# Optimization experiments

Measured on AMD Instinct MI355X. Metric: run time of the kernel, lower is better.

Reference implementation:

```python
import jax, jax.numpy as jnp
import numpy as np
import math

N = 100000      # num vertices
M = 50000       # num hyperedges
NNZ = 800000    # incidence entries
F_IN = 128
NHID = 128
NCLS = 40
DEPTH = 4
ALPHA = 0.1     # restart_alpha
LAMDA = 0.5


def setup_inputs() -> dict:
    key = jax.random.key(0)
    ks = jax.random.split(key, 8)
    x = jax.random.normal(ks[0], (N, F_IN), jnp.float32)
    vertex = jax.random.randint(ks[1], (NNZ,), 0, N)
    edges = jax.random.randint(ks[2], (NNZ,), 0, M)
    s0 = 1.0 / np.sqrt(F_IN)
    sh = 1.0 / np.sqrt(NHID)
    W0 = jax.random.uniform(ks[3], (F_IN, NHID), jnp.float32, -s0, s0)
    b0 = jax.random.uniform(ks[4], (NHID,), jnp.float32, -s0, s0)
    Ws = jax.random.uniform(ks[5], (DEPTH, NHID, NHID), jnp.float32, -sh, sh)
    Wout = jax.random.uniform(ks[6], (NHID, NCLS), jnp.float32, -sh, sh)
    bout = jax.random.uniform(ks[7], (NCLS,), jnp.float32, -sh, sh)
    return {"x": x, "W0": W0, "b0": b0, "Ws": Ws, "Wout": Wout,
            "bout": bout, "vertex": vertex, "edges": edges}


def reference(x, W0, b0, Ws, Wout, bout, vertex, edges):
    ones = jnp.ones((NNZ, 1), x.dtype)
    cnt_e = jnp.maximum(jax.ops.segment_sum(ones, edges, num_segments=M), 1.0)
    cnt_v = jnp.maximum(jax.ops.segment_sum(ones, vertex, num_segments=N), 1.0)

    x = jax.nn.relu(x @ W0 + b0)
    x0 = x
    for i in range(DEPTH):
        beta = math.log(LAMDA / (i + 1) + 1.0)
        # vertex -> edge mean aggregation
        Xve = x[vertex]                                          # [NNZ, NHID]
        Xe = jax.ops.segment_sum(Xve, edges, num_segments=M) / cnt_e
        # edge -> vertex mean aggregation
        Xev = Xe[edges]                                          # [NNZ, NHID]
        Xv = jax.ops.segment_sum(Xev, vertex, num_segments=N) / cnt_v
        # L2 row-normalize with detached scale (use_norm=True)
        norm = jnp.linalg.norm(Xv, axis=1, keepdims=True)
        scale = jax.lax.stop_gradient(jnp.where(norm > 0, 1.0 / norm, 0.0))
        Xv = Xv * scale
        # alpha/beta residual blend (UniGCNII)
        Xi = (1.0 - ALPHA) * Xv + ALPHA * x0
        x = jax.nn.relu((1.0 - beta) * Xi + beta * (Xi @ Ws[i]))
    return x @ Wout + bout
```

## Files before the change

### kernel.cpp

```cpp
#include <hip/hip_runtime.h>

#define NV 100000
#define NE 50000
#define NNZ_C 800000
#define CAP_E 64
#define CAP_V 48
#define NB_E 391
#define NB_V 782
#define CAPB_E 2560
#define CAPB_V 1408
#define OVF_CAP 810000
#define T_ITEMS 2048
#define N_TILES ((NNZ_C + T_ITEMS - 1) / T_ITEMS)

typedef unsigned int uint32;
typedef unsigned short u16;
typedef u16 u16x8 __attribute__((ext_vector_type(8)));
typedef short short8 __attribute__((ext_vector_type(8)));
typedef float floatx16 __attribute__((ext_vector_type(16)));

__device__ __forceinline__ float bf2f(u16 h) {
  return __uint_as_float(((uint32)h) << 16);
}
__device__ __forceinline__ u16 f2bf(float f) {
  uint32 u = __float_as_uint(f);
  u += 0x7FFF + ((u >> 16) & 1);
  return (u16)(u >> 16);
}


__global__ void zero_misc(int* __restrict__ cur, int n,
                          u16* __restrict__ dummyX, u16* __restrict__ dummyXe) {
  int i = blockIdx.x * blockDim.x + threadIdx.x;
  if (i < n) cur[i] = 0;
  if (i < 128) { dummyX[i] = 0; dummyXe[i] = 0; }
}


__global__ __launch_bounds__(256) void scatter_binned(const int* __restrict__ vertex,
                                                      const int* __restrict__ edges,
                                                      int* __restrict__ curE,
                                                      int* __restrict__ curV,
                                                      int* __restrict__ ovfCnt,
                                                      uint32* __restrict__ pairE,
                                                      uint32* __restrict__ pairV,
                                                      uint2* __restrict__ ovfE,
                                                      uint2* __restrict__ ovfV) {
  __shared__ int histE[NB_E], baseE[NB_E];
  __shared__ int histV[NB_V], baseV[NB_V];
  int t = threadIdx.x;
  for (int tile = blockIdx.x; tile < N_TILES; tile += gridDim.x) {
    for (int b = t; b < NB_E; b += 256) histE[b] = 0;
    for (int b = t; b < NB_V; b += 256) histV[b] = 0;
    __syncthreads();
    int base = tile * T_ITEMS;
    int ev[8], vv[8], rE[8], rV[8];
    #pragma unroll
    for (int i = 0; i < 8; i++) {
      int k = base + t + i * 256;
      if (k < NNZ_C) {
        ev[i] = edges[k];
        vv[i] = vertex[k];
        rE[i] = atomicAdd(&histE[ev[i] >> 7], 1);
        rV[i] = atomicAdd(&histV[vv[i] >> 7], 1);
      }
    }
    __syncthreads();
    for (int b = t; b < NB_E; b += 256) {
      int h = histE[b];
      baseE[b] = h ? atomicAdd(&curE[b], h) : 0;
    }
    for (int b = t; b < NB_V; b += 256) {
      int h = histV[b];
      baseV[b] = h ? atomicAdd(&curV[b], h) : 0;
    }
    __syncthreads();
    #pragma unroll
    for (int i = 0; i < 8; i++) {
      int k = base + t + i * 256;
      if (k < NNZ_C) {
        uint32 e = (uint32)ev[i], v = (uint32)vv[i];
        uint32 pkE = ((e & 127u) << 25) | v;
        uint32 pkV = ((v & 127u) << 25) | e;
        int pE = baseE[e >> 7] + rE[i];
        if (pE < CAPB_E) pairE[(size_t)(e >> 7) * CAPB_E + pE] = pkE;
        else { int op = atomicAdd(&ovfCnt[0], 1); if (op < OVF_CAP) ovfE[op] = make_uint2(e >> 7, pkE); }
        int pV = baseV[v >> 7] + rV[i];
        if (pV < CAPB_V) pairV[(size_t)(v >> 7) * CAPB_V + pV] = pkV;
        else { int op = atomicAdd(&ovfCnt[1], 1); if (op < OVF_CAP) ovfV[op] = make_uint2(v >> 7, pkV); }
      }
    }
    __syncthreads();
  }
}

__global__ __launch_bounds__(256) void expand(const uint32* __restrict__ pairs,
                                              const int* __restrict__ cur, int capb,
                                              const uint2* __restrict__ ovf,
                                              const int* __restrict__ ovfCnt,
                                              int* __restrict__ items, int cap,
                                              int* __restrict__ cnt, int nKeys,
                                              int P, int dummy) {
  __shared__ int lcnt[128];
  int b = blockIdx.x, t = threadIdx.x;
  if (t < 128) lcnt[t] = 0;
  __syncthreads();
  int n = min(cur[b], capb);
  const uint32* p = pairs + (size_t)b * capb;
  for (int i = t; i < n; i += 256) {
    uint32 w = p[i];
    int loc = w >> 25;
    int val = (int)(w & 0x1FFFFFFu);
    int r = atomicAdd(&lcnt[loc], 1);
    if (r < cap) items[(size_t)((b << 7) + loc) * cap + r] = val;
  }
  int novf = min(*ovfCnt, OVF_CAP);
  for (int i = t; i < novf; i += 256) {
    uint2 w = ovf[i];
    if ((int)w.x == b) {
      int loc = w.y >> 25;
      int val = (int)(w.y & 0x1FFFFFFu);
      int r = atomicAdd(&lcnt[loc], 1);
      if (r < cap) items[(size_t)((b << 7) + loc) * cap + r] = val;
    }
  }
  __syncthreads();
  if (t < 128) {
    int key = (b << 7) + t;
    if (key < nKeys) {
      int c = lcnt[t];
      cnt[key] = c;
      int cc = min(c, cap);
      int padded = min((max(cc, 1) + P - 1) & ~(P - 1), cap);
      for (int r = cc; r < padded; r++)
        items[(size_t)key * cap + r] = dummy;
    }
  }
}


__global__ void prep_weights(const float* __restrict__ W0, const float* __restrict__ Ws,
                             u16* __restrict__ WT) {
  int idx = blockIdx.x * blockDim.x + threadIdx.x;
  if (idx >= 5 * 16384) return;
  const float betas[4] = {0.4054651081f, 0.2231435513f, 0.1541506798f, 0.1177830357f};
  int sec = idx >> 14;
  int rc = idx & 16383;
  int n = rc >> 7, k = rc & 127;
  float v;
  if (sec == 0) {
    v = W0[k * 128 + n];
  } else {
    int i = sec - 1;
    float b = betas[i];
    v = b * Ws[i * 16384 + k * 128 + n];
    if (k == n) v += 1.0f - b;
  }
  WT[idx] = f2bf(v);
}


__global__ __launch_bounds__(256, 4) void edge_agg(const u16* __restrict__ Xh,
                                                   const int* __restrict__ cntE,
                                                   const int* __restrict__ itemsE,
                                                   u16* __restrict__ Xeh) {
  int g = threadIdx.x >> 4;
  int lane = threadIdx.x & 15;
  int e = blockIdx.x * 16 + g;
  const int* it = itemsE + (size_t)e * CAP_E;
  int4 i0 = *(const int4*)(it);
  int4 i1 = *(const int4*)(it + 4);
  int4 i2 = *(const int4*)(it + 8);
  int4 i3 = *(const int4*)(it + 12);
  int cnt = cntE[e];
  u16x8 r0 = *(const u16x8*)(Xh + (size_t)i0.x * 128 + lane * 8);
  u16x8 r1 = *(const u16x8*)(Xh + (size_t)i0.y * 128 + lane * 8);
  u16x8 r2 = *(const u16x8*)(Xh + (size_t)i0.z * 128 + lane * 8);
  u16x8 r3 = *(const u16x8*)(Xh + (size_t)i0.w * 128 + lane * 8);
  u16x8 r4 = *(const u16x8*)(Xh + (size_t)i1.x * 128 + lane * 8);
  u16x8 r5 = *(const u16x8*)(Xh + (size_t)i1.y * 128 + lane * 8);
  u16x8 r6 = *(const u16x8*)(Xh + (size_t)i1.z * 128 + lane * 8);
  u16x8 r7 = *(const u16x8*)(Xh + (size_t)i1.w * 128 + lane * 8);
  u16x8 r8 = *(const u16x8*)(Xh + (size_t)i2.x * 128 + lane * 8);
  u16x8 r9 = *(const u16x8*)(Xh + (size_t)i2.y * 128 + lane * 8);
  u16x8 rA = *(const u16x8*)(Xh + (size_t)i2.z * 128 + lane * 8);
  u16x8 rB = *(const u16x8*)(Xh + (size_t)i2.w * 128 + lane * 8);
  u16x8 rC = *(const u16x8*)(Xh + (size_t)i3.x * 128 + lane * 8);
  u16x8 rD = *(const u16x8*)(Xh + (size_t)i3.y * 128 + lane * 8);
  u16x8 rE = *(const u16x8*)(Xh + (size_t)i3.z * 128 + lane * 8);
  u16x8 rF = *(const u16x8*)(Xh + (size_t)i3.w * 128 + lane * 8);
  int n16 = (min(cnt, CAP_E) + 15) & ~15;
  int4 p0, p1, p2, p3;
  if (n16 > 16) {
    p0 = *(const int4*)(it + 16);
    p1 = *(const int4*)(it + 20);
    p2 = *(const int4*)(it + 24);
    p3 = *(const int4*)(it + 28);
  }
  float acc[8];
  #pragma unroll
  for (int q = 0; q < 8; q++) {
    float s0 = (bf2f(r0[q]) + bf2f(r1[q])) + (bf2f(r2[q]) + bf2f(r3[q]));
    float s1 = (bf2f(r4[q]) + bf2f(r5[q])) + (bf2f(r6[q]) + bf2f(r7[q]));
    float s2 = (bf2f(r8[q]) + bf2f(r9[q])) + (bf2f(rA[q]) + bf2f(rB[q]));
    float s3 = (bf2f(rC[q]) + bf2f(rD[q])) + (bf2f(rE[q]) + bf2f(rF[q]));
    acc[q] = (s0 + s1) + (s2 + s3);
  }
  int j = 16;
  while (j < n16) {
    u16x8 s0 = *(const u16x8*)(Xh + (size_t)p0.x * 128 + lane * 8);
    u16x8 s1 = *(const u16x8*)(Xh + (size_t)p0.y * 128 + lane * 8);
    u16x8 s2 = *(const u16x8*)(Xh + (size_t)p0.z * 128 + lane * 8);
    u16x8 s3 = *(const u16x8*)(Xh + (size_t)p0.w * 128 + lane * 8);
    u16x8 s4 = *(const u16x8*)(Xh + (size_t)p1.x * 128 + lane * 8);
    u16x8 s5 = *(const u16x8*)(Xh + (size_t)p1.y * 128 + lane * 8);
    u16x8 s6 = *(const u16x8*)(Xh + (size_t)p1.z * 128 + lane * 8);
    u16x8 s7 = *(const u16x8*)(Xh + (size_t)p1.w * 128 + lane * 8);
    u16x8 s8 = *(const u16x8*)(Xh + (size_t)p2.x * 128 + lane * 8);
    u16x8 s9 = *(const u16x8*)(Xh + (size_t)p2.y * 128 + lane * 8);
    u16x8 sA = *(const u16x8*)(Xh + (size_t)p2.z * 128 + lane * 8);
    u16x8 sB = *(const u16x8*)(Xh + (size_t)p2.w * 128 + lane * 8);
    u16x8 sC = *(const u16x8*)(Xh + (size_t)p3.x * 128 + lane * 8);
    u16x8 sD = *(const u16x8*)(Xh + (size_t)p3.y * 128 + lane * 8);
    u16x8 sE = *(const u16x8*)(Xh + (size_t)p3.z * 128 + lane * 8);
    u16x8 sF = *(const u16x8*)(Xh + (size_t)p3.w * 128 + lane * 8);
    j += 16;
    if (j < n16) {
      p0 = *(const int4*)(it + j);
      p1 = *(const int4*)(it + j + 4);
      p2 = *(const int4*)(it + j + 8);
      p3 = *(const int4*)(it + j + 12);
    }
    #pragma unroll
    for (int q = 0; q < 8; q++) {
      float s0x = (bf2f(s0[q]) + bf2f(s1[q])) + (bf2f(s2[q]) + bf2f(s3[q]));
      float s1x = (bf2f(s4[q]) + bf2f(s5[q])) + (bf2f(s6[q]) + bf2f(s7[q]));
      float s2x = (bf2f(s8[q]) + bf2f(s9[q])) + (bf2f(sA[q]) + bf2f(sB[q]));
      float s3x = (bf2f(sC[q]) + bf2f(sD[q])) + (bf2f(sE[q]) + bf2f(sF[q]));
      acc[q] += (s0x + s1x) + (s2x + s3x);
    }
  }
  float inv = 1.f / fmaxf((float)cnt, 1.f);
  u16x8 o;
  #pragma unroll
  for (int q = 0; q < 8; q++) o[q] = f2bf(acc[q] * inv);
  *(u16x8*)(Xeh + (size_t)e * 128 + lane * 8) = o;
}


__global__ __launch_bounds__(256, 5) void gemm_fused(const u16* __restrict__ Xeh,
                                                     const int* __restrict__ cntV,
                                                     const int* __restrict__ itemsV,
                                                     const u16* __restrict__ x0h,
                                                     const u16* __restrict__ WT,
                                                     u16* __restrict__ Yh, int nrows) {
  __shared__ u16 As[32 * 136];
  int t = threadIdx.x;
  int row0 = blockIdx.x * 32;
  int g = t >> 4, lane = t & 15;

  int vcs[2], cnts[2];
  #pragma unroll
  for (int p = 0; p < 2; p++) {
    int v = row0 + p * 16 + g;
    vcs[p] = min(v, nrows - 1);
    cnts[p] = cntV[vcs[p]];
  }
  int4 a0 = *(const int4*)(itemsV + (size_t)vcs[0] * CAP_V);
  int4 a1 = *(const int4*)(itemsV + (size_t)vcs[0] * CAP_V + 4);

  #pragma unroll
  for (int pass = 0; pass < 2; pass++) {
    int v = row0 + pass * 16 + g;
    int vc = vcs[pass];
    int cnt = cnts[pass];
    const int* it = itemsV + (size_t)vc * CAP_V;
    u16x8 r0 = *(const u16x8*)(Xeh + (size_t)a0.x * 128 + lane * 8);
    u16x8 r1 = *(const u16x8*)(Xeh + (size_t)a0.y * 128 + lane * 8);
    u16x8 r2 = *(const u16x8*)(Xeh + (size_t)a0.z * 128 + lane * 8);
    u16x8 r3 = *(const u16x8*)(Xeh + (size_t)a0.w * 128 + lane * 8);
    u16x8 r4 = *(const u16x8*)(Xeh + (size_t)a1.x * 128 + lane * 8);
    u16x8 r5 = *(const u16x8*)(Xeh + (size_t)a1.y * 128 + lane * 8);
    u16x8 r6 = *(const u16x8*)(Xeh + (size_t)a1.z * 128 + lane * 8);
    u16x8 r7 = *(const u16x8*)(Xeh + (size_t)a1.w * 128 + lane * 8);
    u16x8 x0v = *(const u16x8*)(x0h + (size_t)vc * 128 + lane * 8);
    int n8 = (min(cnt, CAP_V) + 7) & ~7;
    int4 b0, b1;
    if (n8 > 8) {
      b0 = *(const int4*)(it + 8);
      b1 = *(const int4*)(it + 12);
    }
    if (pass < 1) {
      const int* itn = itemsV + (size_t)vcs[pass + 1] * CAP_V;
      a0 = *(const int4*)(itn);
      a1 = *(const int4*)(itn + 4);
    }
    float acc[8];
    #pragma unroll
    for (int q = 0; q < 8; q++)
      acc[q] = ((bf2f(r0[q]) + bf2f(r1[q])) + (bf2f(r2[q]) + bf2f(r3[q]))) +
               ((bf2f(r4[q]) + bf2f(r5[q])) + (bf2f(r6[q]) + bf2f(r7[q])));
    int j = 8;
    while (j < n8) {
      u16x8 s0 = *(const u16x8*)(Xeh + (size_t)b0.x * 128 + lane * 8);
      u16x8 s1 = *(const u16x8*)(Xeh + (size_t)b0.y * 128 + lane * 8);
      u16x8 s2 = *(const u16x8*)(Xeh + (size_t)b0.z * 128 + lane * 8);
      u16x8 s3 = *(const u16x8*)(Xeh + (size_t)b0.w * 128 + lane * 8);
      u16x8 s4 = *(const u16x8*)(Xeh + (size_t)b1.x * 128 + lane * 8);
      u16x8 s5 = *(const u16x8*)(Xeh + (size_t)b1.y * 128 + lane * 8);
      u16x8 s6 = *(const u16x8*)(Xeh + (size_t)b1.z * 128 + lane * 8);
      u16x8 s7 = *(const u16x8*)(Xeh + (size_t)b1.w * 128 + lane * 8);
      j += 8;
      if (j < n8) {
        b0 = *(const int4*)(it + j);
        b1 = *(const int4*)(it + j + 4);
      }
      #pragma unroll
      for (int q = 0; q < 8; q++)
        acc[q] += ((bf2f(s0[q]) + bf2f(s1[q])) + (bf2f(s2[q]) + bf2f(s3[q]))) +
                  ((bf2f(s4[q]) + bf2f(s5[q])) + (bf2f(s6[q]) + bf2f(s7[q])));
    }
    float inv = 1.f / fmaxf((float)cnt, 1.f);
    float sq = 0.f;
    #pragma unroll
    for (int q = 0; q < 8; q++) { acc[q] *= inv; sq += acc[q] * acc[q]; }
    sq += __shfl_xor(sq, 1, 64);
    sq += __shfl_xor(sq, 2, 64);
    sq += __shfl_xor(sq, 4, 64);
    sq += __shfl_xor(sq, 8, 64);
    float scale = (sq > 0.f) ? rsqrtf(sq) : 0.f;
    u16x8 o = {0, 0, 0, 0, 0, 0, 0, 0};
    if (v < nrows) {
      #pragma unroll
      for (int q = 0; q < 8; q++)
        o[q] = f2bf(0.9f * acc[q] * scale + 0.1f * bf2f(x0v[q]));
    }
    *(u16x8*)&As[(pass * 16 + g) * 136 + lane * 8] = o;
  }
  __syncthreads();

  int w = t >> 6, lane64 = t & 63;
  int l31 = lane64 & 31, kh = lane64 >> 5;
  floatx16 acc;
  #pragma unroll
  for (int q = 0; q < 16; q++) acc[q] = 0.f;

  const u16* wtb = WT + (size_t)(w * 32 + l31) * 128;
  #pragma unroll
  for (int ks = 0; ks < 8; ks++) {
    int koff = ks * 16 + kh * 8;
    short8 b0 = *(const short8*)(wtb + koff);
    short8 a0 = *(const short8*)&As[l31 * 136 + koff];
    acc = __builtin_amdgcn_mfma_f32_32x32x16_bf16(a0, b0, acc, 0, 0, 0);
  }
  __syncthreads();

  int col = w * 32 + l31;
  #pragma unroll
  for (int reg = 0; reg < 16; reg++) {
    int row = (reg & 3) + 8 * (reg >> 2) + 4 * kh;
    As[row * 136 + col] = f2bf(fmaxf(acc[reg], 0.f));
  }
  __syncthreads();
  #pragma unroll
  for (int i = 0; i < 2; i++) {
    int idx = t + 256 * i;
    int r = idx >> 4, c8 = idx & 15;
    if (row0 + r < nrows)
      *(u16x8*)(Yh + (size_t)(row0 + r) * 128 + c8 * 8) =
          *(const u16x8*)&As[r * 136 + c8 * 8];
  }
}

__global__ __launch_bounds__(256, 4) void gemm_first(const float* __restrict__ A,
                                                     const u16* __restrict__ WT,
                                                     const float* __restrict__ bias,
                                                     u16* __restrict__ Yh,
                                                     u16* __restrict__ Y2h, int nrows) {
  __shared__ u16 As[128 * 136];
  int t = threadIdx.x;
  int row0 = blockIdx.x * 128;
  #pragma unroll
  for (int i = 0; i < 8; i++) {
    int idx = t + 256 * i;
    int r = idx >> 4, c8 = idx & 15;
    u16x8 v = {0, 0, 0, 0, 0, 0, 0, 0};
    if (row0 + r < nrows) {
      const float* p = A + (size_t)(row0 + r) * 128 + c8 * 8;
      float4 a = *(const float4*)p;
      float4 b = *(const float4*)(p + 4);
      v[0] = f2bf(a.x); v[1] = f2bf(a.y); v[2] = f2bf(a.z); v[3] = f2bf(a.w);
      v[4] = f2bf(b.x); v[5] = f2bf(b.y); v[6] = f2bf(b.z); v[7] = f2bf(b.w);
    }
    *(u16x8*)&As[r * 136 + c8 * 8] = v;
  }
  __syncthreads();

  int w = t >> 6, lane = t & 63;
  int l31 = lane & 31, kh = lane >> 5;
  int wr = w >> 1, wc = w & 1;
  floatx16 acc[2][2];
  #pragma unroll
  for (int rt = 0; rt < 2; rt++)
    #pragma unroll
    for (int ct = 0; ct < 2; ct++)
      #pragma unroll
      for (int q = 0; q < 16; q++) acc[rt][ct][q] = 0.f;

  const u16* wtb0 = WT + (size_t)(wc * 64 + l31) * 128;
  const u16* wtb1 = WT + (size_t)(wc * 64 + 32 + l31) * 128;
  #pragma unroll
  for (int ks = 0; ks < 8; ks++) {
    int koff = ks * 16 + kh * 8;
    short8 b0 = *(const short8*)(wtb0 + koff);
    short8 b1 = *(const short8*)(wtb1 + koff);
    short8 a0 = *(const short8*)&As[(wr * 64 + l31) * 136 + koff];
    short8 a1 = *(const short8*)&As[(wr * 64 + 32 + l31) * 136 + koff];
    acc[0][0] = __builtin_amdgcn_mfma_f32_32x32x16_bf16(a0, b0, acc[0][0], 0, 0, 0);
    acc[0][1] = __builtin_amdgcn_mfma_f32_32x32x16_bf16(a0, b1, acc[0][1], 0, 0, 0);
    acc[1][0] = __builtin_amdgcn_mfma_f32_32x32x16_bf16(a1, b0, acc[1][0], 0, 0, 0);
    acc[1][1] = __builtin_amdgcn_mfma_f32_32x32x16_bf16(a1, b1, acc[1][1], 0, 0, 0);
  }
  __syncthreads();

  #pragma unroll
  for (int rt = 0; rt < 2; rt++)
    #pragma unroll
    for (int ct = 0; ct < 2; ct++) {
      int col = wc * 64 + ct * 32 + l31;
      float bv = bias[col];
      #pragma unroll
      for (int reg = 0; reg < 16; reg++) {
        int row = wr * 64 + rt * 32 + (reg & 3) + 8 * (reg >> 2) + 4 * kh;
        As[row * 136 + col] = f2bf(fmaxf(acc[rt][ct][reg] + bv, 0.f));
      }
    }
  __syncthreads();
  #pragma unroll
  for (int i = 0; i < 8; i++) {
    int idx = t + 256 * i;
    int r = idx >> 4, c8 = idx & 15;
    if (row0 + r < nrows) {
      u16x8 v = *(const u16x8*)&As[r * 136 + c8 * 8];
      *(u16x8*)(Yh + (size_t)(row0 + r) * 128 + c8 * 8) = v;
      *(u16x8*)(Y2h + (size_t)(row0 + r) * 128 + c8 * 8) = v;
    }
  }
}


__global__ __launch_bounds__(256) void gemm_out(const u16* __restrict__ Xh,
                                                const float* __restrict__ W,
                                                const float* __restrict__ bias,
                                                float* __restrict__ Y, int nrows) {
  __shared__ float xs[128][36];
  __shared__ float ws[32][44];
  int t = threadIdx.x;
  int tr = t >> 3;
  int tc = t & 7;
  int row0 = blockIdx.x * 128;
  float acc[4][5];
  #pragma unroll
  for (int i = 0; i < 4; i++)
    #pragma unroll
    for (int j = 0; j < 5; j++) acc[i][j] = 0.f;

  for (int k0 = 0; k0 < 128; k0 += 32) {
    #pragma unroll
    for (int i = 0; i < 2; i++) {
      int idx = t + 256 * i;
      int r = idx >> 2, c8 = idx & 3;
      int gr = row0 + r;
      u16x8 v = {0, 0, 0, 0, 0, 0, 0, 0};
      if (gr < nrows) v = *(const u16x8*)(Xh + (size_t)gr * 128 + k0 + c8 * 8);
      #pragma unroll
      for (int q = 0; q < 8; q++) xs[r][c8 * 8 + q] = bf2f(v[q]);
    }
    #pragma unroll
    for (int i = 0; i < 5; i++) {
      int idx = t + 256 * i;
      int r = idx / 40, c = idx % 40;
      ws[r][c] = W[(k0 + r) * 40 + c];
    }
    __syncthreads();
    #pragma unroll
    for (int kk4 = 0; kk4 < 8; kk4++) {
      float4 xv[4];
      #pragma unroll
      for (int i = 0; i < 4; i++) xv[i] = *(const float4*)&xs[tr + 32 * i][kk4 * 4];
      #pragma unroll
      for (int q = 0; q < 4; q++) {
        int kk = kk4 * 4 + q;
        float wv[5];
        #pragma unroll
        for (int j = 0; j < 5; j++) wv[j] = ws[kk][tc * 5 + j];
        #pragma unroll
        for (int i = 0; i < 4; i++) {
          float xq = ((const float*)&xv[i])[q];
          #pragma unroll
          for (int j = 0; j < 5; j++) acc[i][j] += xq * wv[j];
        }
      }
    }
    __syncthreads();
  }
  #pragma unroll
  for (int i = 0; i < 4; i++) {
    int gr = row0 + tr + 32 * i;
    if (gr >= nrows) continue;
    #pragma unroll
    for (int j = 0; j < 5; j++) {
      int c = tc * 5 + j;
      Y[(long)gr * 40 + c] = acc[i][j] + bias[c];
    }
  }
}


extern "C" void kernel_launch(void* const* d_in, const int* in_sizes, int n_in,
                              void* d_out, int out_size, void* d_ws, size_t ws_size,
                              hipStream_t stream) {
  const float* x    = (const float*)d_in[0];
  const float* W0   = (const float*)d_in[1];
  const float* b0   = (const float*)d_in[2];
  const float* Ws   = (const float*)d_in[3];
  const float* Wout = (const float*)d_in[4];
  const float* bout = (const float*)d_in[5];
  const int* vertex = (const int*)d_in[6];
  const int* edges  = (const int*)d_in[7];
  float* out = (float*)d_out;

  char* base = (char*)d_ws;
  size_t o = 0;
  auto alloc = [&](size_t bytes) -> char* {
    char* r = base + o;
    o += (bytes + 255) & ~(size_t)255;
    return r;
  };
  u16* x_curh = (u16*)alloc((size_t)(NV + 1) * 128 * 2);
  u16* x0h    = (u16*)alloc((size_t)NV * 128 * 2);
  u16* Xeh    = (u16*)alloc((size_t)(NE + 1) * 128 * 2);
  u16* WT     = (u16*)alloc((size_t)5 * 16384 * 2);
  int* cntE   = (int*)alloc((size_t)NE * 4);
  int* cntV   = (int*)alloc((size_t)NV * 4);
  int* itemsE = (int*)alloc((size_t)NE * CAP_E * 4);
  int* itemsV = (int*)alloc((size_t)NV * CAP_V * 4);
  uint32* pairE = (uint32*)alloc((size_t)NB_E * CAPB_E * 4);
  uint32* pairV = (uint32*)alloc((size_t)NB_V * CAPB_V * 4);
  uint2* ovfE  = (uint2*)alloc((size_t)OVF_CAP * 8);
  uint2* ovfV  = (uint2*)alloc((size_t)OVF_CAP * 8);
  int* curAll = (int*)alloc((size_t)(NB_E + NB_V + 2) * 4);
  int* curE = curAll;
  int* curV = curAll + NB_E;
  int* ovfCnt = curAll + NB_E + NB_V;

  int nzero = NB_E + NB_V + 2;
  zero_misc<<<(nzero + 255) / 256, 256, 0, stream>>>(curAll, nzero,
                                                     x_curh + (size_t)NV * 128,
                                                     Xeh + (size_t)NE * 128);
  scatter_binned<<<N_TILES, 256, 0, stream>>>(vertex, edges, curE, curV, ovfCnt,
                                              pairE, pairV, ovfE, ovfV);
  expand<<<NB_E, 256, 0, stream>>>(pairE, curE, CAPB_E, ovfE, ovfCnt,
                                   itemsE, CAP_E, cntE, NE, 16, NV);
  expand<<<NB_V, 256, 0, stream>>>(pairV, curV, CAPB_V, ovfV, ovfCnt + 1,
                                   itemsV, CAP_V, cntV, NV, 8, NE);
  prep_weights<<<(5 * 16384 + 255) / 256, 256, 0, stream>>>(W0, Ws, WT);

  int gblocks = (NV + 127) / 128;
  int fblocks = (NV + 31) / 32;
  gemm_first<<<gblocks, 256, 0, stream>>>(x, WT, b0, x_curh, x0h, NV);

  for (int i = 0; i < 4; i++) {
    edge_agg<<<NE / 16, 256, 0, stream>>>(x_curh, cntE, itemsE, Xeh);
    gemm_fused<<<fblocks, 256, 0, stream>>>(Xeh, cntV, itemsV, x0h,
                                            WT + (size_t)(1 + i) * 16384, x_curh, NV);
  }
  gemm_out<<<gblocks, 256, 0, stream>>>(x_curh, Wout, bout, out, NV);
}
```

Measured before the change: 462.1 us.

## Convert edge and vertex aggregation kernels to persistent atomic work-queue scheduling

edge_agg and gemm_fused become persistent kernels launched with a fixed grid. Each wave (edge_agg, 4 edges at a time) or each block (gemm_fused, 32 rows at a time) takes tiles from a global atomic counter, with one counter per layer zeroed at setup. The aim is to balance irregular per-edge and per-vertex degrees across CUs and to avoid tail effects from the large grids. In exchange it adds atomic contention on a single counter, extra block-wide barriers per tile, and the loss of the cross-pass index prefetch in gemm_fused.

New measurement: 1.223 ms. 2.65x slower.

```diff
diff --git a/kernel.cpp b/kernel.cpp
--- a/kernel.cpp
+++ b/kernel.cpp
@@ -12,6 +12,8 @@
 #define OVF_CAP 810000
 #define T_ITEMS 2048
 #define N_TILES ((NNZ_C + T_ITEMS - 1) / T_ITEMS)
+#define FTILES ((NV + 31) / 32)
+#define ETILES (NE / 4)
 
 typedef unsigned int uint32;
 typedef unsigned short u16;
@@ -163,88 +165,96 @@
 __global__ __launch_bounds__(256, 4) void edge_agg(const u16* __restrict__ Xh,
                                                    const int* __restrict__ cntE,
                                                    const int* __restrict__ itemsE,
-                                                   u16* __restrict__ Xeh) {
-  int g = threadIdx.x >> 4;
+                                                   u16* __restrict__ Xeh,
+                                                   int* __restrict__ workCnt) {
+  int wlane = threadIdx.x & 63;
+  int grp = wlane >> 4;
   int lane = threadIdx.x & 15;
-  int e = blockIdx.x * 16 + g;
-  const int* it = itemsE + (size_t)e * CAP_E;
-  int4 i0 = *(const int4*)(it);
-  int4 i1 = *(const int4*)(it + 4);
-  int4 i2 = *(const int4*)(it + 8);
-  int4 i3 = *(const int4*)(it + 12);
-  int cnt = cntE[e];
-  u16x8 r0 = *(const u16x8*)(Xh + (size_t)i0.x * 128 + lane * 8);
-  u16x8 r1 = *(const u16x8*)(Xh + (size_t)i0.y * 128 + lane * 8);
-  u16x8 r2 = *(const u16x8*)(Xh + (size_t)i0.z * 128 + lane * 8);
-  u16x8 r3 = *(const u16x8*)(Xh + (size_t)i0.w * 128 + lane * 8);
-  u16x8 r4 = *(const u16x8*)(Xh + (size_t)i1.x * 128 + lane * 8);
-  u16x8 r5 = *(const u16x8*)(Xh + (size_t)i1.y * 128 + lane * 8);
-  u16x8 r6 = *(const u16x8*)(Xh + (size_t)i1.z * 128 + lane * 8);
-  u16x8 r7 = *(const u16x8*)(Xh + (size_t)i1.w * 128 + lane * 8);
-  u16x8 r8 = *(const u16x8*)(Xh + (size_t)i2.x * 128 + lane * 8);
-  u16x8 r9 = *(const u16x8*)(Xh + (size_t)i2.y * 128 + lane * 8);
-  u16x8 rA = *(const u16x8*)(Xh + (size_t)i2.z * 128 + lane * 8);
-  u16x8 rB = *(const u16x8*)(Xh + (size_t)i2.w * 128 + lane * 8);
-  u16x8 rC = *(const u16x8*)(Xh + (size_t)i3.x * 128 + lane * 8);
-  u16x8 rD = *(const u16x8*)(Xh + (size_t)i3.y * 128 + lane * 8);
-  u16x8 rE = *(const u16x8*)(Xh + (size_t)i3.z * 128 + lane * 8);
-  u16x8 rF = *(const u16x8*)(Xh + (size_t)i3.w * 128 + lane * 8);
-  int n16 = (min(cnt, CAP_E) + 15) & ~15;
-  int4 p0, p1, p2, p3;
-  if (n16 > 16) {
-    p0 = *(const int4*)(it + 16);
-    p1 = *(const int4*)(it + 20);
-    p2 = *(const int4*)(it + 24);
-    p3 = *(const int4*)(it + 28);
-  }
-  float acc[8];
-  #pragma unroll
-  for (int q = 0; q < 8; q++) {
-    float s0 = (bf2f(r0[q]) + bf2f(r1[q])) + (bf2f(r2[q]) + bf2f(r3[q]));
-    float s1 = (bf2f(r4[q]) + bf2f(r5[q])) + (bf2f(r6[q]) + bf2f(r7[q]));
-    float s2 = (bf2f(r8[q]) + bf2f(r9[q])) + (bf2f(rA[q]) + bf2f(rB[q]));
-    float s3 = (bf2f(rC[q]) + bf2f(rD[q])) + (bf2f(rE[q]) + bf2f(rF[q]));
-    acc[q] = (s0 + s1) + (s2 + s3);
-  }
-  int j = 16;
-  while (j < n16) {
-    u16x8 s0 = *(const u16x8*)(Xh + (size_t)p0.x * 128 + lane * 8);
-    u16x8 s1 = *(const u16x8*)(Xh + (size_t)p0.y * 128 + lane * 8);
-    u16x8 s2 = *(const u16x8*)(Xh + (size_t)p0.z * 128 + lane * 8);
-    u16x8 s3 = *(const u16x8*)(Xh + (size_t)p0.w * 128 + lane * 8);
-    u16x8 s4 = *(const u16x8*)(Xh + (size_t)p1.x * 128 + lane * 8);
-    u16x8 s5 = *(const u16x8*)(Xh + (size_t)p1.y * 128 + lane * 8);
-    u16x8 s6 = *(const u16x8*)(Xh + (size_t)p1.z * 128 + lane * 8);
-    u16x8 s7 = *(const u16x8*)(Xh + (size_t)p1.w * 128 + lane * 8);
-    u16x8 s8 = *(const u16x8*)(Xh + (size_t)p2.x * 128 + lane * 8);
-    u16x8 s9 = *(const u16x8*)(Xh + (size_t)p2.y * 128 + lane * 8);
-    u16x8 sA = *(const u16x8*)(Xh + (size_t)p2.z * 128 + lane * 8);
-    u16x8 sB = *(const u16x8*)(Xh + (size_t)p2.w * 128 + lane * 8);
-    u16x8 sC = *(const u16x8*)(Xh + (size_t)p3.x * 128 + lane * 8);
-    u16x8 sD = *(const u16x8*)(Xh + (size_t)p3.y * 128 + lane * 8);
-    u16x8 sE = *(const u16x8*)(Xh + (size_t)p3.z * 128 + lane * 8);
-    u16x8 sF = *(const u16x8*)(Xh + (size_t)p3.w * 128 + lane * 8);
-    j += 16;
-    if (j < n16) {
-      p0 = *(const int4*)(it + j);
-      p1 = *(const int4*)(it + j + 4);
-      p2 = *(const int4*)(it + j + 8);
-      p3 = *(const int4*)(it + j + 12);
-    }
+  for (;;) {
+    int tile = 0;
+    if (wlane == 0) tile = atomicAdd(workCnt, 1);
+    tile = __shfl(tile, 0, 64);
+    if (tile >= ETILES) break;
+    int e = tile * 4 + grp;
+    const int* it = itemsE + (size_t)e * CAP_E;
+    int4 i0 = *(const int4*)(it);
+    int4 i1 = *(const int4*)(it + 4);
+    int4 i2 = *(const int4*)(it + 8);
+    int4 i3 = *(const int4*)(it + 12);
+    int cnt = cntE[e];
+    u16x8 r0 = *(const u16x8*)(Xh + (size_t)i0.x * 128 + lane * 8);
+    u16x8 r1 = *(const u16x8*)(Xh + (size_t)i0.y * 128 + lane * 8);
+    u16x8 r2 = *(const u16x8*)(Xh + (size_t)i0.z * 128 + lane * 8);
+    u16x8 r3 = *(const u16x8*)(Xh + (size_t)i0.w * 128 + lane * 8);
+    u16x8 r4 = *(const u16x8*)(Xh + (size_t)i1.x * 128 + lane * 8);
+    u16x8 r5 = *(const u16x8*)(Xh + (size_t)i1.y * 128 + lane * 8);
+    u16x8 r6 = *(const u16x8*)(Xh + (size_t)i1.z * 128 + lane * 8);
+    u16x8 r7 = *(const u16x8*)(Xh + (size_t)i1.w * 128 + lane * 8);
+    u16x8 r8 = *(const u16x8*)(Xh + (size_t)i2.x * 128 + lane * 8);
+    u16x8 r9 = *(const u16x8*)(Xh + (size_t)i2.y * 128 + lane * 8);
+    u16x8 rA = *(const u16x8*)(Xh + (size_t)i2.z * 128 + lane * 8);
+    u16x8 rB = *(const u16x8*)(Xh + (size_t)i2.w * 128 + lane * 8);
+    u16x8 rC = *(const u16x8*)(Xh + (size_t)i3.x * 128 + lane * 8);
+    u16x8 rD = *(const u16x8*)(Xh + (size_t)i3.y * 128 + lane * 8);
+    u16x8 rE = *(const u16x8*)(Xh + (size_t)i3.z * 128 + lane * 8);
+    u16x8 rF = *(const u16x8*)(Xh + (size_t)i3.w * 128 + lane * 8);
+    int n16 = (min(cnt, CAP_E) + 15) & ~15;
+    int4 p0, p1, p2, p3;
+    if (n16 > 16) {
+      p0 = *(const int4*)(it + 16);
+      p1 = *(const int4*)(it + 20);
+      p2 = *(const int4*)(it + 24);
+      p3 = *(const int4*)(it + 28);
+    }
+    float acc[8];
     #pragma unroll
     for (int q = 0; q < 8; q++) {
-      float s0x = (bf2f(s0[q]) + bf2f(s1[q])) + (bf2f(s2[q]) + bf2f(s3[q]));
-      float s1x = (bf2f(s4[q]) + bf2f(s5[q])) + (bf2f(s6[q]) + bf2f(s7[q]));
-      float s2x = (bf2f(s8[q]) + bf2f(s9[q])) + (bf2f(sA[q]) + bf2f(sB[q]));
-      float s3x = (bf2f(sC[q]) + bf2f(sD[q])) + (bf2f(sE[q]) + bf2f(sF[q]));
-      acc[q] += (s0x + s1x) + (s2x + s3x);
-    }
-  }
-  float inv = 1.f / fmaxf((float)cnt, 1.f);
-  u16x8 o;
-  #pragma unroll
-  for (int q = 0; q < 8; q++) o[q] = f2bf(acc[q] * inv);
-  *(u16x8*)(Xeh + (size_t)e * 128 + lane * 8) = o;
+      float s0 = (bf2f(r0[q]) + bf2f(r1[q])) + (bf2f(r2[q]) + bf2f(r3[q]));
+      float s1 = (bf2f(r4[q]) + bf2f(r5[q])) + (bf2f(r6[q]) + bf2f(r7[q]));
+      float s2 = (bf2f(r8[q]) + bf2f(r9[q])) + (bf2f(rA[q]) + bf2f(rB[q]));
+      float s3 = (bf2f(rC[q]) + bf2f(rD[q])) + (bf2f(rE[q]) + bf2f(rF[q]));
+      acc[q] = (s0 + s1) + (s2 + s3);
+    }
+    int j = 16;
+    while (j < n16) {
+      u16x8 s0 = *(const u16x8*)(Xh + (size_t)p0.x * 128 + lane * 8);
+      u16x8 s1 = *(const u16x8*)(Xh + (size_t)p0.y * 128 + lane * 8);
+      u16x8 s2 = *(const u16x8*)(Xh + (size_t)p0.z * 128 + lane * 8);
+      u16x8 s3 = *(const u16x8*)(Xh + (size_t)p0.w * 128 + lane * 8);
+      u16x8 s4 = *(const u16x8*)(Xh + (size_t)p1.x * 128 + lane * 8);
+      u16x8 s5 = *(const u16x8*)(Xh + (size_t)p1.y * 128 + lane * 8);
+      u16x8 s6 = *(const u16x8*)(Xh + (size_t)p1.z * 128 + lane * 8);
+      u16x8 s7 = *(const u16x8*)(Xh + (size_t)p1.w * 128 + lane * 8);
+      u16x8 s8 = *(const u16x8*)(Xh + (size_t)p2.x * 128 + lane * 8);
+      u16x8 s9 = *(const u16x8*)(Xh + (size_t)p2.y * 128 + lane * 8);
+      u16x8 sA = *(const u16x8*)(Xh + (size_t)p2.z * 128 + lane * 8);
+      u16x8 sB = *(const u16x8*)(Xh + (size_t)p2.w * 128 + lane * 8);
+      u16x8 sC = *(const u16x8*)(Xh + (size_t)p3.x * 128 + lane * 8);
+      u16x8 sD = *(const u16x8*)(Xh + (size_t)p3.y * 128 + lane * 8);
+      u16x8 sE = *(const u16x8*)(Xh + (size_t)p3.z * 128 + lane * 8);
+      u16x8 sF = *(const u16x8*)(Xh + (size_t)p3.w * 128 + lane * 8);
+      j += 16;
+      if (j < n16) {
+        p0 = *(const int4*)(it + j);
+        p1 = *(const int4*)(it + j + 4);
+        p2 = *(const int4*)(it + j + 8);
+        p3 = *(const int4*)(it + j + 12);
+      }
+      #pragma unroll
+      for (int q = 0; q < 8; q++) {
+        float s0x = (bf2f(s0[q]) + bf2f(s1[q])) + (bf2f(s2[q]) + bf2f(s3[q]));
+        float s1x = (bf2f(s4[q]) + bf2f(s5[q])) + (bf2f(s6[q]) + bf2f(s7[q]));
+        float s2x = (bf2f(s8[q]) + bf2f(s9[q])) + (bf2f(sA[q]) + bf2f(sB[q]));
+        float s3x = (bf2f(sC[q]) + bf2f(sD[q])) + (bf2f(sE[q]) + bf2f(sF[q]));
+        acc[q] += (s0x + s1x) + (s2x + s3x);
+      }
+    }
+    float inv = 1.f / fmaxf((float)cnt, 1.f);
+    u16x8 o;
+    #pragma unroll
+    for (int q = 0; q < 8; q++) o[q] = f2bf(acc[q] * inv);
+    *(u16x8*)(Xeh + (size_t)e * 128 + lane * 8) = o;
+  }
 }
 
 
@@ -253,122 +263,115 @@
                                                      const int* __restrict__ itemsV,
                                                      const u16* __restrict__ x0h,
                                                      const u16* __restrict__ WT,
-                                                     u16* __restrict__ Yh, int nrows) {
+                                                     u16* __restrict__ Yh, int nrows,
+                                                     int* __restrict__ workCnt) {
   __shared__ u16 As[32 * 136];
+  __shared__ int s_tile;
   int t = threadIdx.x;
-  int row0 = blockIdx.x * 32;
   int g = t >> 4, lane = t & 15;
-
-  int vcs[2], cnts[2];
-  #pragma unroll
-  for (int p = 0; p < 2; p++) {
-    int v = row0 + p * 16 + g;
-    vcs[p] = min(v, nrows - 1);
-    cnts[p] = cntV[vcs[p]];
-  }
-  int4 a0 = *(const int4*)(itemsV + (size_t)vcs[0] * CAP_V);
-  int4 a1 = *(const int4*)(itemsV + (size_t)vcs[0] * CAP_V + 4);
-
-  #pragma unroll
-  for (int pass = 0; pass < 2; pass++) {
-    int v = row0 + pass * 16 + g;
-    int vc = vcs[pass];
-    int cnt = cnts[pass];
-    const int* it = itemsV + (size_t)vc * CAP_V;
-    u16x8 r0 = *(const u16x8*)(Xeh + (size_t)a0.x * 128 + lane * 8);
-    u16x8 r1 = *(const u16x8*)(Xeh + (size_t)a0.y * 128 + lane * 8);
-    u16x8 r2 = *(const u16x8*)(Xeh + (size_t)a0.z * 128 + lane * 8);
-    u16x8 r3 = *(const u16x8*)(Xeh + (size_t)a0.w * 128 + lane * 8);
-    u16x8 r4 = *(const u16x8*)(Xeh + (size_t)a1.x * 128 + lane * 8);
-    u16x8 r5 = *(const u16x8*)(Xeh + (size_t)a1.y * 128 + lane * 8);
-    u16x8 r6 = *(const u16x8*)(Xeh + (size_t)a1.z * 128 + lane * 8);
-    u16x8 r7 = *(const u16x8*)(Xeh + (size_t)a1.w * 128 + lane * 8);
-    u16x8 x0v = *(const u16x8*)(x0h + (size_t)vc * 128 + lane * 8);
-    int n8 = (min(cnt, CAP_V) + 7) & ~7;
-    int4 b0, b1;
-    if (n8 > 8) {
-      b0 = *(const int4*)(it + 8);
-      b1 = *(const int4*)(it + 12);
-    }
-    if (pass < 1) {
-      const int* itn = itemsV + (size_t)vcs[pass + 1] * CAP_V;
-      a0 = *(const int4*)(itn);
-      a1 = *(const int4*)(itn + 4);
-    }
-    float acc[8];
-    #pragma unroll
-    for (int q = 0; q < 8; q++)
-      acc[q] = ((bf2f(r0[q]) + bf2f(r1[q])) + (bf2f(r2[q]) + bf2f(r3[q]))) +
-               ((bf2f(r4[q]) + bf2f(r5[q])) + (bf2f(r6[q]) + bf2f(r7[q])));
-    int j = 8;
-    while (j < n8) {
-      u16x8 s0 = *(const u16x8*)(Xeh + (size_t)b0.x * 128 + lane * 8);
-      u16x8 s1 = *(const u16x8*)(Xeh + (size_t)b0.y * 128 + lane * 8);
-      u16x8 s2 = *(const u16x8*)(Xeh + (size_t)b0.z * 128 + lane * 8);
-      u16x8 s3 = *(const u16x8*)(Xeh + (size_t)b0.w * 128 + lane * 8);
-      u16x8 s4 = *(const u16x8*)(Xeh + (size_t)b1.x * 128 + lane * 8);
-      u16x8 s5 = *(const u16x8*)(Xeh + (size_t)b1.y * 128 + lane * 8);
-      u16x8 s6 = *(const u16x8*)(Xeh + (size_t)b1.z * 128 + lane * 8);
-      u16x8 s7 = *(const u16x8*)(Xeh + (size_t)b1.w * 128 + lane * 8);
-      j += 8;
-      if (j < n8) {
-        b0 = *(const int4*)(it + j);
-        b1 = *(const int4*)(it + j + 4);
-      }
+  int w = t >> 6, lane64 = t & 63;
+  int l31 = lane64 & 31, kh = lane64 >> 5;
+
+  for (;;) {
+    if (t == 0) s_tile = atomicAdd(workCnt, 1);
+    __syncthreads();
+    int tile = s_tile;
+    if (tile >= FTILES) break;
+    int row0 = tile * 32;
+
+    #pragma unroll
+    for (int pass = 0; pass < 2; pass++) {
+      int v = row0 + pass * 16 + g;
+      const int* it = itemsV + (size_t)v * CAP_V;
+      int4 a0 = *(const int4*)(it);
+      int4 a1 = *(const int4*)(it + 4);
+      int cnt = cntV[v];
+      u16x8 r0 = *(const u16x8*)(Xeh + (size_t)a0.x * 128 + lane * 8);
+      u16x8 r1 = *(const u16x8*)(Xeh + (size_t)a0.y * 128 + lane * 8);
+      u16x8 r2 = *(const u16x8*)(Xeh + (size_t)a0.z * 128 + lane * 8);
+      u16x8 r3 = *(const u16x8*)(Xeh + (size_t)a0.w * 128 + lane * 8);
+      u16x8 r4 = *(const u16x8*)(Xeh + (size_t)a1.x * 128 + lane * 8);
+      u16x8 r5 = *(const u16x8*)(Xeh + (size_t)a1.y * 128 + lane * 8);
+      u16x8 r6 = *(const u16x8*)(Xeh + (size_t)a1.z * 128 + lane * 8);
+      u16x8 r7 = *(const u16x8*)(Xeh + (size_t)a1.w * 128 + lane * 8);
+      u16x8 x0v = *(const u16x8*)(x0h + (size_t)v * 128 + lane * 8);
+      int n8 = (min(cnt, CAP_V) + 7) & ~7;
+      int4 b0, b1;
+      if (n8 > 8) {
+        b0 = *(const int4*)(it + 8);
+        b1 = *(const int4*)(it + 12);
+      }
+      float acc[8];
       #pragma unroll
       for (int q = 0; q < 8; q++)
-        acc[q] += ((bf2f(s0[q]) + bf2f(s1[q])) + (bf2f(s2[q]) + bf2f(s3[q]))) +
-                  ((bf2f(s4[q]) + bf2f(s5[q])) + (bf2f(s6[q]) + bf2f(s7[q])));
-    }
-    float inv = 1.f / fmaxf((float)cnt, 1.f);
-    float sq = 0.f;
-    #pragma unroll
-    for (int q = 0; q < 8; q++) { acc[q] *= inv; sq += acc[q] * acc[q]; }
-    sq += __shfl_xor(sq, 1, 64);
-    sq += __shfl_xor(sq, 2, 64);
-    sq += __shfl_xor(sq, 4, 64);
-    sq += __shfl_xor(sq, 8, 64);
-    float scale = (sq > 0.f) ? rsqrtf(sq) : 0.f;
-    u16x8 o = {0, 0, 0, 0, 0, 0, 0, 0};
-    if (v < nrows) {
+        acc[q] = ((bf2f(r0[q]) + bf2f(r1[q])) + (bf2f(r2[q]) + bf2f(r3[q]))) +
+                 ((bf2f(r4[q]) + bf2f(r5[q])) + (bf2f(r6[q]) + bf2f(r7[q])));
+      int j = 8;
+      while (j < n8) {
+        u16x8 s0 = *(const u16x8*)(Xeh + (size_t)b0.x * 128 + lane * 8);
+        u16x8 s1 = *(const u16x8*)(Xeh + (size_t)b0.y * 128 + lane * 8);
+        u16x8 s2 = *(const u16x8*)(Xeh + (size_t)b0.z * 128 + lane * 8);
+        u16x8 s3 = *(const u16x8*)(Xeh + (size_t)b0.w * 128 + lane * 8);
+        u16x8 s4 = *(const u16x8*)(Xeh + (size_t)b1.x * 128 + lane * 8);
+        u16x8 s5 = *(const u16x8*)(Xeh + (size_t)b1.y * 128 + lane * 8);
+        u16x8 s6 = *(const u16x8*)(Xeh + (size_t)b1.z * 128 + lane * 8);
+        u16x8 s7 = *(const u16x8*)(Xeh + (size_t)b1.w * 128 + lane * 8);
+        j += 8;
+        if (j < n8) {
+          b0 = *(const int4*)(it + j);
+          b1 = *(const int4*)(it + j + 4);
+        }
+        #pragma unroll
+        for (int q = 0; q < 8; q++)
+          acc[q] += ((bf2f(s0[q]) + bf2f(s1[q])) + (bf2f(s2[q]) + bf2f(s3[q]))) +
+                    ((bf2f(s4[q]) + bf2f(s5[q])) + (bf2f(s6[q]) + bf2f(s7[q])));
+      }
+      float inv = 1.f / fmaxf((float)cnt, 1.f);
+      float sq = 0.f;
+      #pragma unroll
+      for (int q = 0; q < 8; q++) { acc[q] *= inv; sq += acc[q] * acc[q]; }
+      sq += __shfl_xor(sq, 1, 64);
+      sq += __shfl_xor(sq, 2, 64);
+      sq += __shfl_xor(sq, 4, 64);
+      sq += __shfl_xor(sq, 8, 64);
+      float scale = (sq > 0.f) ? rsqrtf(sq) : 0.f;
+      u16x8 o;
       #pragma unroll
       for (int q = 0; q < 8; q++)
         o[q] = f2bf(0.9f * acc[q] * scale + 0.1f * bf2f(x0v[q]));
-    }
-    *(u16x8*)&As[(pass * 16 + g) * 136 + lane * 8] = o;
-  }
-  __syncthreads();
-
-  int w = t >> 6, lane64 = t & 63;
-  int l31 = lane64 & 31, kh = lane64 >> 5;
-  floatx16 acc;
-  #pragma unroll
-  for (int q = 0; q < 16; q++) acc[q] = 0.f;
-
-  const u16* wtb = WT + (size_t)(w * 32 + l31) * 128;
-  #pragma unroll
-  for (int ks = 0; ks < 8; ks++) {
-    int koff = ks * 16 + kh * 8;
-    short8 b0 = *(const short8*)(wtb + koff);
-    short8 a0 = *(const short8*)&As[l31 * 136 + koff];
-    acc = __builtin_amdgcn_mfma_f32_32x32x16_bf16(a0, b0, acc, 0, 0, 0);
-  }
-  __syncthreads();
-
-  int col = w * 32 + l31;
-  #pragma unroll
-  for (int reg = 0; reg < 16; reg++) {
-    int row = (reg & 3) + 8 * (reg >> 2) + 4 * kh;
-    As[row * 136 + col] = f2bf(fmaxf(acc[reg], 0.f));
-  }
-  __syncthreads();
-  #pragma unroll
-  for (int i = 0; i < 2; i++) {
-    int idx = t + 256 * i;
-    int r = idx >> 4, c8 = idx & 15;
-    if (row0 + r < nrows)
+      *(u16x8*)&As[(pass * 16 + g) * 136 + lane * 8] = o;
+    }
+    __syncthreads();
+
+    floatx16 acc;
+    #pragma unroll
+    for (int q = 0; q < 16; q++) acc[q] = 0.f;
+
+    const u16* wtb = WT + (size_t)(w * 32 + l31) * 128;
+    #pragma unroll
+    for (int ks = 0; ks < 8; ks++) {
+      int koff = ks * 16 + kh * 8;
+      short8 b0 = *(const short8*)(wtb + koff);
+      short8 a0 = *(const short8*)&As[l31 * 136 + koff];
+      acc = __builtin_amdgcn_mfma_f32_32x32x16_bf16(a0, b0, acc, 0, 0, 0);
+    }
+    __syncthreads();
+
+    int col = w * 32 + l31;
+    #pragma unroll
+    for (int reg = 0; reg < 16; reg++) {
+      int row = (reg & 3) + 8 * (reg >> 2) + 4 * kh;
+      As[row * 136 + col] = f2bf(fmaxf(acc[reg], 0.f));
+    }
+    __syncthreads();
+    #pragma unroll
+    for (int i = 0; i < 2; i++) {
+      int idx = t + 256 * i;
+      int r = idx >> 4, c8 = idx & 15;
       *(u16x8*)(Yh + (size_t)(row0 + r) * 128 + c8 * 8) =
           *(const u16x8*)&As[r * 136 + c8 * 8];
+    }
+    __syncthreads();
   }
 }
 
@@ -549,12 +552,13 @@
   uint32* pairV = (uint32*)alloc((size_t)NB_V * CAPB_V * 4);
   uint2* ovfE  = (uint2*)alloc((size_t)OVF_CAP * 8);
   uint2* ovfV  = (uint2*)alloc((size_t)OVF_CAP * 8);
-  int* curAll = (int*)alloc((size_t)(NB_E + NB_V + 2) * 4);
+  int* curAll = (int*)alloc((size_t)(NB_E + NB_V + 10) * 4);
   int* curE = curAll;
   int* curV = curAll + NB_E;
   int* ovfCnt = curAll + NB_E + NB_V;
-
-  int nzero = NB_E + NB_V + 2;
+  int* wq = curAll + NB_E + NB_V + 2;
+
+  int nzero = NB_E + NB_V + 10;
   zero_misc<<<(nzero + 255) / 256, 256, 0, stream>>>(curAll, nzero,
                                                      x_curh + (size_t)NV * 128,
                                                      Xeh + (size_t)NE * 128);
@@ -567,13 +571,13 @@
   prep_weights<<<(5 * 16384 + 255) / 256, 256, 0, stream>>>(W0, Ws, WT);
 
   int gblocks = (NV + 127) / 128;
-  int fblocks = (NV + 31) / 32;
   gemm_first<<<gblocks, 256, 0, stream>>>(x, WT, b0, x_curh, x0h, NV);
 
   for (int i = 0; i < 4; i++) {
-    edge_agg<<<NE / 16, 256, 0, stream>>>(x_curh, cntE, itemsE, Xeh);
-    gemm_fused<<<fblocks, 256, 0, stream>>>(Xeh, cntV, itemsV, x0h,
-                                            WT + (size_t)(1 + i) * 16384, x_curh, NV);
+    edge_agg<<<1024, 256, 0, stream>>>(x_curh, cntE, itemsE, Xeh, wq + i);
+    gemm_fused<<<1280, 256, 0, stream>>>(Xeh, cntV, itemsV, x0h,
+                                         WT + (size_t)(1 + i) * 16384, x_curh, NV,
+                                         wq + 4 + i);
   }
   gemm_out<<<gblocks, 256, 0, stream>>>(x_curh, Wout, bout, out, NV);
 }
```
